# Kernel optimization log

Measured on AMD Instinct MI355X. Metric: run time of the kernel, lower is better.

## Reference

```python
import jax, jax.numpy as jnp
import numpy as np
from jax.scipy.optimize import minimize

LAMDA = 0.01        # lamda default in MI()
N_DOMAINS = 2       # domain_label is binary (source/target)
MAXITER = 50        # BFGS iteration budget (torchmin l-bfgs analogue)


def _sq_dists(A, B):
    # squared euclidean pairwise distances == torch.cdist(A, B, p=2) ** 2
    an = jnp.sum(A * A, axis=-1)
    bn = jnp.sum(B * B, axis=-1)
    return an[:, None] + bn[None, :] - 2.0 * (A @ B.T)


def _median_sigma(sf):
    # sigma = median of nonzero squared pairwise source distances.
    # With continuous features the only zeros are the diagonal, so mask it.
    pd = jnp.maximum(_sq_dists(sf, sf), 0.0)
    pd = jnp.where(jnp.eye(pd.shape[0], dtype=bool), jnp.nan, pd)
    return jnp.nanmedian(pd)


def _build(sf, tf, y, l):
    # Gaussian kernel masked by class agreement, plus domain one-hots.
    sigma = _median_sigma(sf)
    X = jnp.concatenate([sf, tf], axis=0)              # [N, d]
    D = _sq_dists(X, X)                                 # [N, N]
    Deltay = (y[:, None] == y[None, :]).astype(X.dtype)
    K_W = jnp.exp(-D / sigma) * Deltay                  # [N, N]
    onehot = jax.nn.one_hot(l[:, 0], N_DOMAINS, dtype=X.dtype)  # [N, 2]
    KD = K_W * (onehot @ onehot.T)                      # K_W * Deltal
    w = jnp.sum(onehot, axis=0) / X.shape[0]            # domain counts / N
    return K_W, KD, onehot, w


def _div(theta, K_W, KD, onehot, w):
    # mean((K_W*Deltal) @ theta) - mean(exp((theta*K_W) @ Deltal - 1))
    # Deltal = onehot @ onehot.T (rank-2), so the second NxN @ NxN matmul
    # collapses to A = K_W @ (theta[:,None]*onehot) with column weights w.
    term1 = jnp.mean(KD @ theta)
    A = K_W @ (theta[:, None] * onehot)                 # [N, 2]
    term2 = jnp.mean(jnp.exp(A - 1.0) @ w)
    return term1 - term2


def _solve_theta(K_W, KD, onehot, w):
    N = K_W.shape[0]
    obj = lambda th: -_div(th, K_W, KD, onehot, w) + LAMDA * (th @ th)
    res = minimize(obj, jnp.zeros((N,), K_W.dtype), method="BFGS",
                   options={"maxiter": MAXITER})
    return res.x


def setup_inputs() -> dict:
    key = jax.random.key(0)
    k1, k2, k3, k4 = jax.random.split(key, 4)
    B, d, n_class = 2048, 256, 31
    source_features = jax.random.normal(k1, (B, d), dtype=jnp.float32)
    target_features = jax.random.normal(k2, (B, d), dtype=jnp.float32)
    y = jax.random.randint(k3, (2 * B,), 0, n_class, dtype=jnp.int32)
    l = jax.random.randint(k4, (2 * B, 1), 0, N_DOMAINS, dtype=jnp.int32)
    return {"source_features": source_features, "target_features": target_features,
            "y": y, "l": l}


def reference(source_features, target_features, y, l):
    K_W, KD, onehot, w = _build(source_features, target_features, y, l)
    theta_hat = _solve_theta(K_W, KD, onehot, w)
    return _div(theta_hat, K_W, KD, onehot, w)
```

## Files before the change

### kernel.cpp

```cpp
#include <hip/hip_runtime.h>
#include <math.h>

#define N_TOT   4096
#define N_SRC   2048
#define DIMF    256
#define NCLASS  31
#define LAMBDA  0.01f

#define K_TRI1  1048063LL
#define K_TRI2  1048064LL

#define WS_ACC    0
#define WS_HIST0  64
#define WS_HISTA  16448
#define WS_HISTB  32832
#define WS_H2A    49216
#define WS_H2B    50240
#define WS_STATE  51264
#define WS_TICK   51520
#define WS_META   52288
#define WS_SCAL   52800
#define ZERO_BYTES 53248
#define WS_PERM   53248
#define WS_XN     69632
#define WS_DS     1048576
#define WS_KBLK   17825792

#define MAXW 224
#define MAXM 112
#define WPAD 114

__device__ __forceinline__ float bf2f(unsigned short h) {
  return __uint_as_float(((unsigned)h) << 16);
}

__device__ __forceinline__ double blockReduceSum(double v, double* red) {
#pragma unroll
  for (int o = 32; o > 0; o >>= 1) v += __shfl_down(v, o, 64);
  int w = threadIdx.x >> 6, lane = threadIdx.x & 63;
  __syncthreads();
  if (lane == 0) red[w] = v;
  __syncthreads();
  return red[0] + red[1] + red[2] + red[3];
}

__device__ __forceinline__ void blockReduceSumMax(double s, double mx, double* red,
                                                  double& os, double& om) {
#pragma unroll
  for (int o = 32; o > 0; o >>= 1) {
    s += __shfl_down(s, o, 64);
    double u = __shfl_down(mx, o, 64);
    mx = fmax(mx, u);
  }
  int w = threadIdx.x >> 6, lane = threadIdx.x & 63;
  __syncthreads();
  if (lane == 0) { red[w] = s; red[4 + w] = mx; }
  __syncthreads();
  os = red[0] + red[1] + red[2] + red[3];
  om = fmax(fmax(red[4], red[5]), fmax(red[6], red[7]));
}

__device__ void scan_find(const unsigned* hist, int nbins, long long k, unsigned* shOut) {
  __shared__ long long tsum[256];
  int tid = threadIdx.x;
  int per = nbins / 256;
  long long s = 0;
  for (int q = 0; q < per; q++) s += hist[tid * per + q];
  tsum[tid] = s;
  __syncthreads();
  if (tid == 0) {
    long long run = 0;
    for (int t = 0; t < 256; t++) { long long v = tsum[t]; tsum[t] = run; run += v; }
  }
  __syncthreads();
  long long run = tsum[tid];
  for (int q = 0; q < per; q++) {
    unsigned c = hist[tid * per + q];
    if (k >= run && k < run + (long long)c) { shOut[0] = (unsigned)(tid * per + q); shOut[1] = (unsigned)(k - run); }
    run += c;
  }
  __syncthreads();
}

__global__ __launch_bounds__(256) void xn_kernel(const float* __restrict__ sf,
                                                 const float* __restrict__ tf,
                                                 float* __restrict__ xn) {
  int wid = threadIdx.x >> 6, lane = threadIdx.x & 63;
  int row = blockIdx.x * 4 + wid;
  const float* src = (row < N_SRC) ? (sf + (size_t)row * DIMF) : (tf + (size_t)(row - N_SRC) * DIMF);
  float4 v = ((const float4*)src)[lane];
  float s = v.x * v.x + v.y * v.y + v.z * v.z + v.w * v.w;
#pragma unroll
  for (int o = 32; o > 0; o >>= 1) s += __shfl_down(s, o, 64);
  if (lane == 0) xn[row] = s;
}

__global__ __launch_bounds__(256) void dist_k(const float* __restrict__ sf,
                                              const float* __restrict__ xn,
                                              float* __restrict__ Ds,
                                              unsigned* __restrict__ h) {
  __shared__ float As[16][68];
  __shared__ float Bs[16][68];
  __shared__ unsigned lh[4096];
  const int tx = threadIdx.x, ty = threadIdx.y;
  const int tid = ty * 16 + tx;
  for (int q = tid; q < 4096; q += 256) lh[q] = 0;
  int b = blockIdx.x;
  int by = (int)((sqrtf(8.f * (float)b + 1.f) - 1.f) * 0.5f);
  while ((by + 1) * (by + 2) / 2 <= b) ++by;
  while (by * (by + 1) / 2 > b) --by;
  int bx = b - by * (by + 1) / 2;
  const int R = by * 64, C = bx * 64;
  const int si = tid >> 2, sq = tid & 3;
  float4 va = ((const float4*)(sf + (size_t)(R + si) * 256 + 0))[sq];
  float4 vb = ((const float4*)(sf + (size_t)(C + si) * 256 + 0))[sq];
  float acc[4][4] = {};
  for (int kc = 0; kc < 256; kc += 16) {
    As[sq * 4 + 0][si] = va.x; As[sq * 4 + 1][si] = va.y; As[sq * 4 + 2][si] = va.z; As[sq * 4 + 3][si] = va.w;
    Bs[sq * 4 + 0][si] = vb.x; Bs[sq * 4 + 1][si] = vb.y; Bs[sq * 4 + 2][si] = vb.z; Bs[sq * 4 + 3][si] = vb.w;
    __syncthreads();
    if (kc + 16 < 256) {
      va = ((const float4*)(sf + (size_t)(R + si) * 256 + kc + 16))[sq];
      vb = ((const float4*)(sf + (size_t)(C + si) * 256 + kc + 16))[sq];
    }
#pragma unroll
    for (int k = 0; k < 16; k++) {
      float4 a = *(const float4*)&As[k][ty * 4];
      float4 b2 = *(const float4*)&Bs[k][tx * 4];
      acc[0][0] += a.x * b2.x; acc[0][1] += a.x * b2.y; acc[0][2] += a.x * b2.z; acc[0][3] += a.x * b2.w;
      acc[1][0] += a.y * b2.x; acc[1][1] += a.y * b2.y; acc[1][2] += a.y * b2.z; acc[1][3] += a.y * b2.w;
      acc[2][0] += a.z * b2.x; acc[2][1] += a.z * b2.y; acc[2][2] += a.z * b2.z; acc[2][3] += a.z * b2.w;
      acc[3][0] += a.w * b2.x; acc[3][1] += a.w * b2.y; acc[3][2] += a.w * b2.z; acc[3][3] += a.w * b2.w;
    }
    __syncthreads();
  }
  int jbase = C + tx * 4;
  float xnj0 = xn[jbase + 0], xnj1 = xn[jbase + 1], xnj2 = xn[jbase + 2], xnj3 = xn[jbase + 3];
#pragma unroll
  for (int r = 0; r < 4; r++) {
    int i = R + ty * 4 + r;
    float xni = xn[i];
    float v[4];
    v[0] = fmaxf(xni + xnj0 - 2.f * acc[r][0], 0.f);
    v[1] = fmaxf(xni + xnj1 - 2.f * acc[r][1], 0.f);
    v[2] = fmaxf(xni + xnj2 - 2.f * acc[r][2], 0.f);
    v[3] = fmaxf(xni + xnj3 - 2.f * acc[r][3], 0.f);
    if (jbase + 3 < i) {
      float4 o; o.x = v[0]; o.y = v[1]; o.z = v[2]; o.w = v[3];
      ((float4*)&Ds[(size_t)i * 2048 + jbase])[0] = o;
      atomicAdd(&lh[__float_as_uint(v[0]) >> 20], 1u);
      atomicAdd(&lh[__float_as_uint(v[1]) >> 20], 1u);
      atomicAdd(&lh[__float_as_uint(v[2]) >> 20], 1u);
      atomicAdd(&lh[__float_as_uint(v[3]) >> 20], 1u);
    } else {
#pragma unroll
      for (int k = 0; k < 4; k++) {
        if (jbase + k < i) {
          Ds[(size_t)i * 2048 + jbase + k] = v[k];
          atomicAdd(&lh[__float_as_uint(v[k]) >> 20], 1u);
        }
      }
    }
  }
  __syncthreads();
  for (int q = tid; q < 4096; q += 256) if (lh[q]) atomicAdd(&h[q], lh[q]);
}

__global__ __launch_bounds__(256) void scan0_k(const unsigned* __restrict__ h, unsigned* __restrict__ st) {
  __shared__ unsigned r0[2];
  __shared__ unsigned r1[2];
  scan_find(h, 4096, K_TRI1, r0);
  scan_find(h, 4096, K_TRI2, r1);
  if (threadIdx.x == 0) { st[0] = r0[0]; st[1] = r0[1]; st[2] = r1[0]; st[3] = r1[1]; }
}

__global__ __launch_bounds__(256) void hist1_k(const float* __restrict__ Ds, const unsigned* __restrict__ st,
                                               unsigned* __restrict__ hA, unsigned* __restrict__ hB) {
  __shared__ unsigned lA[4096];
  __shared__ unsigned lB[4096];
  for (int i = threadIdx.x; i < 4096; i += 256) { lA[i] = 0; lB[i] = 0; }
  __syncthreads();
  unsigned s0 = st[0], s1 = st[2];
  int gw = (blockIdx.x * 256 + threadIdx.x) >> 6;
  int lane = threadIdx.x & 63;
  const float* row = Ds + (size_t)gw * 2048;
  for (int j = lane; j < gw; j += 64) {
    unsigned u = __float_as_uint(row[j]);
    unsigned hi = u >> 20, mid = (u >> 8) & 0xFFFu;
    if (hi == s0) atomicAdd(&lA[mid], 1u);
    if (hi == s1) atomicAdd(&lB[mid], 1u);
  }
  __syncthreads();
  for (int i = threadIdx.x; i < 4096; i += 256) {
    if (lA[i]) atomicAdd(&hA[i], lA[i]);
    if (lB[i]) atomicAdd(&hB[i], lB[i]);
  }
}

__global__ __launch_bounds__(256) void scan1_k(const unsigned* __restrict__ hA, const unsigned* __restrict__ hB,
                                               unsigned* __restrict__ st) {
  __shared__ unsigned r0[2];
  __shared__ unsigned r1[2];
  long long kA = (long long)st[1];
  long long kB = (long long)st[3];
  scan_find(hA, 4096, kA, r0);
  scan_find(hB, 4096, kB, r1);
  if (threadIdx.x == 0) { st[4] = r0[0]; st[5] = r0[1]; st[6] = r1[0]; st[7] = r1[1]; }
}

__global__ __launch_bounds__(256) void hist2_k(const float* __restrict__ Ds, const unsigned* __restrict__ st,
                                               unsigned* __restrict__ hA, unsigned* __restrict__ hB) {
  __shared__ unsigned lA[256];
  __shared__ unsigned lB[256];
  lA[threadIdx.x] = 0; lB[threadIdx.x] = 0;
  __syncthreads();
  unsigned p0 = (st[0] << 12) | st[4];
  unsigned p1 = (st[2] << 12) | st[6];
  int gw = (blockIdx.x * 256 + threadIdx.x) >> 6;
  int lane = threadIdx.x & 63;
  const float* row = Ds + (size_t)gw * 2048;
  for (int j = lane; j < gw; j += 64) {
    unsigned u = __float_as_uint(row[j]);
    unsigned pre = u >> 8;
    if (pre == p0) atomicAdd(&lA[u & 0xFFu], 1u);
    if (pre == p1) atomicAdd(&lB[u & 0xFFu], 1u);
  }
  __syncthreads();
  if (lA[threadIdx.x]) atomicAdd(&hA[threadIdx.x], lA[threadIdx.x]);
  if (lB[threadIdx.x]) atomicAdd(&hB[threadIdx.x], lB[threadIdx.x]);
}

__global__ __launch_bounds__(256) void scan2b_k(const unsigned* __restrict__ hA, const unsigned* __restrict__ hB,
                                                const unsigned* __restrict__ st, float* __restrict__ scal,
                                                const int* __restrict__ y, const int* __restrict__ l,
                                                int* __restrict__ perm, int* __restrict__ meta) {
  int tid = threadIdx.x;
  __shared__ unsigned r0[2];
  __shared__ unsigned r1[2];
  scan_find(hA, 256, (long long)st[5], r0);
  scan_find(hB, 256, (long long)st[7], r1);
  if (tid == 0) {
    unsigned v1 = (st[0] << 20) | (st[4] << 8) | r0[0];
    unsigned v2 = (st[2] << 20) | (st[6] << 8) | r1[0];
    scal[0] = 0.5f * (__uint_as_float(v1) + __uint_as_float(v2));
  }
  __shared__ unsigned cl[64];
  __shared__ unsigned bs2[64];
  __shared__ unsigned cur[64];
  if (tid < 64) cl[tid] = 0;
  __syncthreads();
  for (int i = tid; i < N_TOT; i += 256) atomicAdd(&cl[y[i] * 2 + l[i]], 1u);
  __syncthreads();
  if (tid == 0) {
    unsigned run = 0;
    for (int b2 = 0; b2 < 62; b2++) { bs2[b2] = run; run += cl[b2]; }
    unsigned run2 = 0, cnt0 = 0;
    for (int c = 0; c < NCLASS; c++) {
      int n = (int)(cl[2 * c] + cl[2 * c + 1]);
      meta[c] = n; meta[32 + c] = (int)cl[2 * c]; meta[64 + c] = (int)bs2[2 * c];
      meta[96 + c] = (int)run2; run2 += (unsigned)(n * n);
      cnt0 += cl[2 * c];
    }
    scal[1] = (float)((double)cnt0 / (4096.0 * 4096.0));
    scal[2] = (float)((double)(N_TOT - cnt0) / (4096.0 * 4096.0));
  }
  __syncthreads();
  if (tid < 64) cur[tid] = bs2[tid];
  __syncthreads();
  for (int i = tid; i < N_TOT; i += 256) {
    int b2 = y[i] * 2 + l[i];
    unsigned pos = atomicAdd(&cur[b2], 1u);
    perm[pos] = i;
  }
}

__global__ __launch_bounds__(256) void build_k(const float* __restrict__ sf, const float* __restrict__ tf,
                                               const float* __restrict__ xn, const int* __restrict__ perm,
                                               const int* __restrict__ meta, const float* __restrict__ scal,
                                               float* __restrict__ gK) {
  const int c = blockIdx.z;
  const int n = meta[c];
  const int cs = meta[64 + c];
  const int bo = meta[96 + c];
  const int T = (n + 15) >> 4;
  int b = blockIdx.x;
  if (b >= T * (T + 1) / 2) return;
  int by = (int)((sqrtf(8.f * (float)b + 1.f) - 1.f) * 0.5f);
  while ((by + 1) * (by + 2) / 2 <= b) ++by;
  while (by * (by + 1) / 2 > b) --by;
  int bx = b - by * (by + 1) / 2;
  const int i0 = by * 16, j0 = bx * 16;
  const int tx = threadIdx.x, ty = threadIdx.y;
  __shared__ float As[16][260];
  __shared__ float Bs[16][260];
  __shared__ float ot[16][17];
  __shared__ int ra[16];
  __shared__ int rb[16];
  int tid = ty * 16 + tx;
  if (tid < 16) { int il = i0 + tid; ra[tid] = (il < n) ? perm[cs + il] : -1; }
  else if (tid < 32) { int jl = j0 + tid - 16; rb[tid - 16] = (jl < n) ? perm[cs + jl] : -1; }
  __syncthreads();
  for (int e = tid; e < 1024; e += 256) {
    int r = e >> 6, q = e & 63;
    int g = ra[r];
    if (g >= 0) {
      const float* src = (g < N_SRC) ? (sf + (size_t)g * DIMF) : (tf + (size_t)(g - N_SRC) * DIMF);
      ((float4*)&As[r][q * 4])[0] = ((const float4*)src)[q];
    }
    int g2 = rb[r];
    if (g2 >= 0) {
      const float* src = (g2 < N_SRC) ? (sf + (size_t)g2 * DIMF) : (tf + (size_t)(g2 - N_SRC) * DIMF);
      ((float4*)&Bs[r][q * 4])[0] = ((const float4*)src)[q];
    }
  }
  __syncthreads();
  int il = i0 + ty, jl = j0 + tx;
  float val = 0.f;
  if (il < n && jl < n) {
    float dot = 0.f;
    const float4* a4 = (const float4*)&As[ty][0];
    const float4* b4 = (const float4*)&Bs[tx][0];
#pragma unroll 16
    for (int q = 0; q < 64; q++) {
      float4 a = a4[q], b2 = b4[q];
      dot += a.x * b2.x + a.y * b2.y + a.z * b2.z + a.w * b2.w;
    }
    int gi = ra[ty], gj = rb[tx];
    float d = xn[gi] + xn[gj] - 2.f * dot;
    val = expf(-d / scal[0]);
    gK[(size_t)bo + (size_t)il * n + jl] = val;
  }
  ot[ty][tx] = val;
  __syncthreads();
  if (by != bx) {
    int il2 = j0 + ty, jl2 = i0 + tx;
    if (il2 < n && jl2 < n) gK[(size_t)bo + (size_t)il2 * n + jl2] = ot[tx][ty];
  }
}

__global__ __launch_bounds__(256) void solver_k(const float* __restrict__ gK, const int* __restrict__ meta,
                                                const float* __restrict__ scal, double* __restrict__ acc,
                                                unsigned* __restrict__ tick, float* __restrict__ out) {
  const int c = blockIdx.x >> 1, d = blockIdx.x & 1;
  const int n = meta[c];
  const int m0 = meta[32 + c];
  const int m = d ? (n - m0) : m0;
  const int c0 = d ? m0 : 0;
  const int bo = meta[96 + c];
  const float gamma = scal[1 + d];
  const int tid = threadIdx.x;
  const int wv = tid >> 6, lane = tid & 63;

  __shared__ unsigned short Wl[MAXW * WPAD];
  __shared__ float pS[4 * MAXM];
  __shared__ float pD[4 * MAXM];
  __shared__ float Av[MAXW];
  __shared__ float Sv[MAXW];
  __shared__ float Uv[MAXW];
  __shared__ float Bq[MAXW];
  __shared__ float bc[MAXM];
  __shared__ float th[MAXM + 1];
  __shared__ float gv[MAXM];
  __shared__ float dgv[MAXM];
  __shared__ float pv[MAXM + 1];
  __shared__ float rv[MAXM + 1];
  __shared__ float zv[MAXM + 1];
  __shared__ float xv[MAXM + 1];
  __shared__ double red[16];

  const float* K = gK + bo;
  const int st = n;
  const int mp2 = (m + 1) & ~1;
  const int iw0 = (n * wv) >> 2, iw1 = (n * (wv + 1)) >> 2;

  for (int i = tid >> 2; i < n; i += 64) {
    const float* Kr = K + (size_t)i * st + c0;
    unsigned short* Wr = Wl + i * WPAD;
    for (int j = (tid & 3); j < m; j += 4) {
      unsigned u = __float_as_uint(Kr[j]);
      u += 0x7fffu + ((u >> 16) & 1u);
      Wr[j] = (unsigned short)(u >> 16);
    }
    if ((tid & 3) == 0 && (m & 1)) Wr[m] = 0;
  }
  {
    const int r0 = (m * wv) >> 2, r1 = (m * (wv + 1)) >> 2;
    for (int j = lane; j < m; j += 64) {
      const float* Kr = K + (size_t)(c0 + j) * st + c0;
      float s = 0.f;
      for (int r = r0; r < r1; r++) s += Kr[r];
      pS[wv * MAXM + j] = s;
    }
  }
  __syncthreads();
  for (int j = tid; j < mp2; j += 256) {
    if (j < m) bc[j] = (pS[j] + pS[MAXM + j] + pS[2 * MAXM + j] + pS[3 * MAXM + j]) * (1.0f / 4096.0f);
    th[j] = 0.f;
  }
  __syncthreads();

  for (int it = 0; it < 25; it++) {
    double o = 0.0;
    if (it == 0) {
      const float s0c = gamma * expf(-1.f);
      for (int i = tid; i < n; i += 256) { Av[i] = 0.f; Sv[i] = s0c; o += (double)s0c; }
    } else {
      for (int i = tid; i < n; i += 256) {
        const unsigned short* Wr = Wl + i * WPAD;
        float a = 0.f;
#pragma unroll 4
        for (int j = 0; j < mp2; j += 2) {
          unsigned u = *(const unsigned*)(Wr + j);
          a += __uint_as_float(u << 16) * th[j]
             + __uint_as_float(u & 0xffff0000u) * th[j + 1];
        }
        Av[i] = a;
      }
      __syncthreads();
      for (int i = tid; i < n; i += 256) {
        float si = gamma * expf(fminf(Av[i] - 1.f, 30.f));
        Sv[i] = si; o += (double)si;
      }
      for (int j = tid; j < m; j += 256) {
        float t_ = th[j];
        o += (double)(-bc[j] * t_ + LAMBDA * t_ * t_);
      }
    }
    __syncthreads();
    if (it == 0) {
      for (int j = lane; j < m; j += 64) {
        const unsigned short* Wc = Wl + j;
        float s_ = 0.f, ds_ = 0.f;
        int i = iw0;
        for (; i + 3 < iw1; i += 4) {
          float w0 = bf2f(Wc[(i + 0) * WPAD]), w1 = bf2f(Wc[(i + 1) * WPAD]);
          float w2 = bf2f(Wc[(i + 2) * WPAD]), w3 = bf2f(Wc[(i + 3) * WPAD]);
          float a0 = w0 * Sv[i], a1 = w1 * Sv[i + 1], a2 = w2 * Sv[i + 2], a3 = w3 * Sv[i + 3];
          s_ += a0 + a1 + a2 + a3;
          ds_ += a0 * w0 + a1 * w1 + a2 * w2 + a3 * w3;
        }
        for (; i < iw1; i++) { float w = bf2f(Wc[i * WPAD]); float a = w * Sv[i]; s_ += a; ds_ += a * w; }
        pS[wv * MAXM + j] = s_; pD[wv * MAXM + j] = ds_;
      }
    } else {
      for (int j = lane; j < m; j += 64) {
        const unsigned short* Wc = Wl + j;
        float s_ = 0.f;
        int i = iw0;
        for (; i + 3 < iw1; i += 4)
          s_ += bf2f(Wc[(i+0)*WPAD]) * Sv[i]   + bf2f(Wc[(i+1)*WPAD]) * Sv[i+1]
              + bf2f(Wc[(i+2)*WPAD]) * Sv[i+2] + bf2f(Wc[(i+3)*WPAD]) * Sv[i+3];
        for (; i < iw1; i++) s_ += bf2f(Wc[i * WPAD]) * Sv[i];
        pS[wv * MAXM + j] = s_;
      }
    }
    __syncthreads();
    double gm = 0.0;
    for (int j = tid; j < m; j += 256) {
      float s_ = pS[j] + pS[MAXM + j] + pS[2 * MAXM + j] + pS[3 * MAXM + j];
      if (it == 0) {
        float ds_ = pD[j] + pD[MAXM + j] + pD[2 * MAXM + j] + pD[3 * MAXM + j];
        dgv[j] = ds_ + 2.f * LAMBDA;
      }
      float g = s_ - bc[j] + 2.f * LAMBDA * th[j];
      gv[j] = g;
      double ag = fabs((double)g); if (ag > gm) gm = ag;
    }
    double obj, gmax;
    blockReduceSumMax(o, gm, red, obj, gmax);
    if (gmax < 1e-5) break;

    const double tolf = (it == 0) ? 1e-2 : ((it == 1) ? 1e-3 : 1e-4);
    double rz = 0.0;
    for (int j = tid; j < mp2; j += 256) {
      float r0 = (j < m) ? -gv[j] : 0.f;
      float z0 = (j < m) ? r0 / dgv[j] : 0.f;
      rv[j] = r0; zv[j] = z0; pv[j] = z0; xv[j] = 0.f;
      rz += (double)r0 * (double)z0;
    }
    rz = blockReduceSum(rz, red);
    double rz0 = rz;
    for (int cg = 0; cg < 12; cg++) {
      __syncthreads();
      for (int i = tid; i < n; i += 256) {
        const unsigned short* Wr = Wl + i * WPAD;
        float a = 0.f;
#pragma unroll 4
        for (int j = 0; j < mp2; j += 2) {
          unsigned u = *(const unsigned*)(Wr + j);
          a += __uint_as_float(u << 16) * pv[j]
             + __uint_as_float(u & 0xffff0000u) * pv[j + 1];
        }
        Uv[i] = a * Sv[i];
      }
      __syncthreads();
      for (int j = lane; j < m; j += 64) {
        const unsigned short* Wc = Wl + j;
        float q = 0.f;
        int i = iw0;
        for (; i + 3 < iw1; i += 4)
          q += bf2f(Wc[(i+0)*WPAD]) * Uv[i]   + bf2f(Wc[(i+1)*WPAD]) * Uv[i+1]
             + bf2f(Wc[(i+2)*WPAD]) * Uv[i+2] + bf2f(Wc[(i+3)*WPAD]) * Uv[i+3];
        for (; i < iw1; i++) q += bf2f(Wc[i * WPAD]) * Uv[i];
        pS[wv * MAXM + j] = q;
      }
      __syncthreads();
      double pq = 0.0;
      for (int j = tid; j < m; j += 256) {
        float q = pS[j] + pS[MAXM + j] + pS[2 * MAXM + j] + pS[3 * MAXM + j] + 2.f * LAMBDA * pv[j];
        Bq[j] = q;
        pq += (double)pv[j] * (double)q;
      }
      pq = blockReduceSum(pq, red);
      if (!(pq > 0.0)) break;
      float alpha = (float)(rz / pq);
      double rznew = 0.0;
      for (int j = tid; j < m; j += 256) {
        xv[j] += alpha * pv[j];
        float rn = rv[j] - alpha * Bq[j];
        rv[j] = rn;
        float zn = rn / dgv[j];
        zv[j] = zn;
        rznew += (double)rn * (double)zn;
      }
      rznew = blockReduceSum(rznew, red);
      if (rznew < tolf * rz0 || cg == 11) break;
      float beta = (float)(rznew / rz);
      for (int j = tid; j < m; j += 256) pv[j] = zv[j] + beta * pv[j];
      rz = rznew;
    }
    __syncthreads();
    double gtpl = 0.0, pml = 0.0;
    for (int j = tid; j < m; j += 256) {
      gtpl += (double)gv[j] * (double)xv[j];
      double ax = fabs((double)xv[j]); if (ax > pml) pml = ax;
    }
    double gtp, pmax;
    blockReduceSumMax(gtpl, pml, red, gtp, pmax);
    if (!(gtp < 0.0)) break;

    float t = 1.f;
    if (-gtp >= 1e-4) {
      for (int i = tid; i < n; i += 256) {
        const unsigned short* Wr = Wl + i * WPAD;
        float a = 0.f;
#pragma unroll 4
        for (int j = 0; j < mp2; j += 2) {
          unsigned u = *(const unsigned*)(Wr + j);
          a += __uint_as_float(u << 16) * xv[j]
             + __uint_as_float(u & 0xffff0000u) * xv[j + 1];
        }
        Bq[i] = a;
      }
      __syncthreads();
      for (int ls = 0; ls < 10; ls++) {
        double ol = 0.0;
        for (int i = tid; i < n; i += 256)
          ol += (double)(gamma * expf(fminf(Av[i] + t * Bq[i] - 1.f, 30.f)));
        for (int j = tid; j < m; j += 256) {
          float tj = th[j] + t * xv[j];
          ol += (double)(-bc[j] * tj + LAMBDA * tj * tj);
        }
        double ot2 = blockReduceSum(ol, red);
        if (ot2 <= obj + 1e-4 * (double)t * gtp) break;
        t *= 0.5f;
      }
    }
    for (int j = tid; j < mp2; j += 256) th[j] += t * xv[j];
    __syncthreads();
    if ((double)t * pmax < 1e-7) break;
  }

  __syncthreads();
  for (int i = tid; i < n; i += 256) {
    const float* Kr = K + (size_t)i * st + c0;
    float a = 0.f;
    int j = 0;
    for (; j + 7 < m; j += 8)
      a += th[j] * Kr[j] + th[j+1] * Kr[j+1] + th[j+2] * Kr[j+2] + th[j+3] * Kr[j+3]
         + th[j+4] * Kr[j+4] + th[j+5] * Kr[j+5] + th[j+6] * Kr[j+6] + th[j+7] * Kr[j+7];
    for (; j < m; j++) a += th[j] * Kr[j];
    Av[i] = a;
  }
  __syncthreads();
  double t1l = 0.0, t2l = 0.0;
  for (int i = tid; i < n; i += 256) t2l += (double)(gamma * expf(fminf(Av[i] - 1.f, 30.f)));
  for (int j = tid; j < m; j += 256) t1l += (double)(bc[j] * th[j]);
  double t1 = blockReduceSum(t1l, red);
  double t2 = blockReduceSum(t2l, red);
  if (tid == 0) {
    atomicAdd(&acc[0], t1);
    atomicAdd(&acc[1], t2);
    __threadfence();
    unsigned old = __hip_atomic_fetch_add(&tick[0], 1u, __ATOMIC_ACQ_REL, __HIP_MEMORY_SCOPE_AGENT);
    if (old == 61u) {
      double a0 = __hip_atomic_load(&acc[0], __ATOMIC_RELAXED, __HIP_MEMORY_SCOPE_AGENT);
      double a1 = __hip_atomic_load(&acc[1], __ATOMIC_RELAXED, __HIP_MEMORY_SCOPE_AGENT);
      out[0] = (float)(a0 - a1);
    }
  }
}

extern "C" void kernel_launch(void* const* d_in, const int* in_sizes, int n_in,
                              void* d_out, int out_size, void* d_ws, size_t ws_size,
                              hipStream_t stream) {
  const float* sf = (const float*)d_in[0];
  const float* tf = (const float*)d_in[1];
  const int* y = (const int*)d_in[2];
  const int* l = (const int*)d_in[3];
  char* ws = (char*)d_ws;

  double*   acc    = (double*)(ws + WS_ACC);
  unsigned* hist0  = (unsigned*)(ws + WS_HIST0);
  unsigned* histA  = (unsigned*)(ws + WS_HISTA);
  unsigned* histB  = (unsigned*)(ws + WS_HISTB);
  unsigned* h2A    = (unsigned*)(ws + WS_H2A);
  unsigned* h2B    = (unsigned*)(ws + WS_H2B);
  unsigned* state  = (unsigned*)(ws + WS_STATE);
  unsigned* tick   = (unsigned*)(ws + WS_TICK);
  int*      meta   = (int*)(ws + WS_META);
  float*    scal   = (float*)(ws + WS_SCAL);
  int*      perm   = (int*)(ws + WS_PERM);
  float*    xnp    = (float*)(ws + WS_XN);
  float*    Ds     = (float*)(ws + WS_DS);
  float*    gK     = (float*)(ws + WS_KBLK);

  hipMemsetAsync(d_ws, 0, ZERO_BYTES, stream);
  hipLaunchKernelGGL(xn_kernel, dim3(1024), dim3(256), 0, stream, sf, tf, xnp);
  hipLaunchKernelGGL(dist_k, dim3(528), dim3(16, 16), 0, stream, sf, xnp, Ds, hist0);
  hipLaunchKernelGGL(scan0_k, dim3(1), dim3(256), 0, stream, hist0, state);
  hipLaunchKernelGGL(hist1_k, dim3(512), dim3(256), 0, stream, Ds, state, histA, histB);
  hipLaunchKernelGGL(scan1_k, dim3(1), dim3(256), 0, stream, histA, histB, state);
  hipLaunchKernelGGL(hist2_k, dim3(512), dim3(256), 0, stream, Ds, state, h2A, h2B);
  hipLaunchKernelGGL(scan2b_k, dim3(1), dim3(256), 0, stream, h2A, h2B, state, scal, y, l, perm, meta);
  hipLaunchKernelGGL(build_k, dim3(105, 1, NCLASS), dim3(16, 16), 0, stream, sf, tf, xnp, perm, meta, scal, gK);
  hipLaunchKernelGGL(solver_k, dim3(62), dim3(256), 0, stream, gK, meta, scal, acc, tick, (float*)d_out);
}
```

Measured before the change: 232.5 us.

## Fuse radix-select refinement passes and shrink solver blocks to two waves

```diff
diff --git a/kernel.cpp b/kernel.cpp
--- a/kernel.cpp
+++ b/kernel.cpp
@@ -14,8 +14,6 @@
 #define WS_HIST0  64
 #define WS_HISTA  16448
 #define WS_HISTB  32832
-#define WS_H2A    49216
-#define WS_H2B    50240
 #define WS_STATE  51264
 #define WS_TICK   51520
 #define WS_META   52288
@@ -25,6 +23,8 @@
 #define WS_XN     69632
 #define WS_DS     1048576
 #define WS_KBLK   17825792
+#define WS_BIGA   17825792
+#define WS_BIGB   22020096
 
 #define MAXW 224
 #define MAXM 112
@@ -34,18 +34,18 @@
   return __uint_as_float(((unsigned)h) << 16);
 }
 
-__device__ __forceinline__ double blockReduceSum(double v, double* red) {
+__device__ __forceinline__ double blockReduceSum2(double v, double* red) {
 #pragma unroll
   for (int o = 32; o > 0; o >>= 1) v += __shfl_down(v, o, 64);
   int w = threadIdx.x >> 6, lane = threadIdx.x & 63;
   __syncthreads();
   if (lane == 0) red[w] = v;
   __syncthreads();
-  return red[0] + red[1] + red[2] + red[3];
-}
-
-__device__ __forceinline__ void blockReduceSumMax(double s, double mx, double* red,
-                                                  double& os, double& om) {
+  return red[0] + red[1];
+}
+
+__device__ __forceinline__ void blockReduceSumMax2(double s, double mx, double* red,
+                                                   double& os, double& om) {
 #pragma unroll
   for (int o = 32; o > 0; o >>= 1) {
     s += __shfl_down(s, o, 64);
@@ -56,8 +56,8 @@
   __syncthreads();
   if (lane == 0) { red[w] = s; red[4 + w] = mx; }
   __syncthreads();
-  os = red[0] + red[1] + red[2] + red[3];
-  om = fmax(fmax(red[4], red[5]), fmax(red[6], red[7]));
+  os = red[0] + red[1];
+  om = fmax(red[4], red[5]);
 }
 
 __device__ void scan_find(const unsigned* hist, int nbins, long long k, unsigned* shOut) {
@@ -98,12 +98,17 @@
 __global__ __launch_bounds__(256) void dist_k(const float* __restrict__ sf,
                                               const float* __restrict__ xn,
                                               float* __restrict__ Ds,
-                                              unsigned* __restrict__ h) {
+                                              unsigned* __restrict__ h,
+                                              uint4* __restrict__ bigz) {
   __shared__ float As[16][68];
   __shared__ float Bs[16][68];
   __shared__ unsigned lh[4096];
   const int tx = threadIdx.x, ty = threadIdx.y;
   const int tid = ty * 16 + tx;
+  {
+    uint4 z; z.x = 0; z.y = 0; z.z = 0; z.w = 0;
+    for (int q = blockIdx.x * 256 + tid; q < 524288; q += 135168) bigz[q] = z;
+  }
   for (int q = tid; q < 4096; q += 256) lh[q] = 0;
   int b = blockIdx.x;
   int by = (int)((sqrtf(8.f * (float)b + 1.f) - 1.f) * 0.5f);
@@ -175,7 +180,8 @@
 }
 
 __global__ __launch_bounds__(256) void hist1_k(const float* __restrict__ Ds, const unsigned* __restrict__ st,
-                                               unsigned* __restrict__ hA, unsigned* __restrict__ hB) {
+                                               unsigned* __restrict__ hA, unsigned* __restrict__ hB,
+                                               unsigned* __restrict__ bigA, unsigned* __restrict__ bigB) {
   __shared__ unsigned lA[4096];
   __shared__ unsigned lB[4096];
   for (int i = threadIdx.x; i < 4096; i += 256) { lA[i] = 0; lB[i] = 0; }
@@ -187,8 +193,8 @@
   for (int j = lane; j < gw; j += 64) {
     unsigned u = __float_as_uint(row[j]);
     unsigned hi = u >> 20, mid = (u >> 8) & 0xFFFu;
-    if (hi == s0) atomicAdd(&lA[mid], 1u);
-    if (hi == s1) atomicAdd(&lB[mid], 1u);
+    if (hi == s0) { atomicAdd(&lA[mid], 1u); atomicAdd(&bigA[u & 0xFFFFFu], 1u); }
+    if (hi == s1) { atomicAdd(&lB[mid], 1u); atomicAdd(&bigB[u & 0xFFFFFu], 1u); }
   }
   __syncthreads();
   for (int i = threadIdx.x; i < 4096; i += 256) {
@@ -197,51 +203,20 @@
   }
 }
 
-__global__ __launch_bounds__(256) void scan1_k(const unsigned* __restrict__ hA, const unsigned* __restrict__ hB,
-                                               unsigned* __restrict__ st) {
-  __shared__ unsigned r0[2];
-  __shared__ unsigned r1[2];
-  long long kA = (long long)st[1];
-  long long kB = (long long)st[3];
-  scan_find(hA, 4096, kA, r0);
-  scan_find(hB, 4096, kB, r1);
-  if (threadIdx.x == 0) { st[4] = r0[0]; st[5] = r0[1]; st[6] = r1[0]; st[7] = r1[1]; }
-}
-
-__global__ __launch_bounds__(256) void hist2_k(const float* __restrict__ Ds, const unsigned* __restrict__ st,
-                                               unsigned* __restrict__ hA, unsigned* __restrict__ hB) {
-  __shared__ unsigned lA[256];
-  __shared__ unsigned lB[256];
-  lA[threadIdx.x] = 0; lB[threadIdx.x] = 0;
-  __syncthreads();
-  unsigned p0 = (st[0] << 12) | st[4];
-  unsigned p1 = (st[2] << 12) | st[6];
-  int gw = (blockIdx.x * 256 + threadIdx.x) >> 6;
-  int lane = threadIdx.x & 63;
-  const float* row = Ds + (size_t)gw * 2048;
-  for (int j = lane; j < gw; j += 64) {
-    unsigned u = __float_as_uint(row[j]);
-    unsigned pre = u >> 8;
-    if (pre == p0) atomicAdd(&lA[u & 0xFFu], 1u);
-    if (pre == p1) atomicAdd(&lB[u & 0xFFu], 1u);
-  }
-  __syncthreads();
-  if (lA[threadIdx.x]) atomicAdd(&hA[threadIdx.x], lA[threadIdx.x]);
-  if (lB[threadIdx.x]) atomicAdd(&hB[threadIdx.x], lB[threadIdx.x]);
-}
-
-__global__ __launch_bounds__(256) void scan2b_k(const unsigned* __restrict__ hA, const unsigned* __restrict__ hB,
-                                                const unsigned* __restrict__ st, float* __restrict__ scal,
-                                                const int* __restrict__ y, const int* __restrict__ l,
-                                                int* __restrict__ perm, int* __restrict__ meta) {
+__global__ __launch_bounds__(256) void scanF_k(const unsigned* __restrict__ hA, const unsigned* __restrict__ hB,
+                                               const unsigned* __restrict__ bigA, const unsigned* __restrict__ bigB,
+                                               const unsigned* __restrict__ st, float* __restrict__ scal,
+                                               const int* __restrict__ y, const int* __restrict__ l,
+                                               int* __restrict__ perm, int* __restrict__ meta) {
   int tid = threadIdx.x;
-  __shared__ unsigned r0[2];
-  __shared__ unsigned r1[2];
-  scan_find(hA, 256, (long long)st[5], r0);
-  scan_find(hB, 256, (long long)st[7], r1);
+  __shared__ unsigned m0[2], m1[2], l0[2], l1[2];
+  scan_find(hA, 4096, (long long)st[1], m0);
+  scan_find(hB, 4096, (long long)st[3], m1);
+  scan_find(bigA + (size_t)m0[0] * 256, 256, (long long)m0[1], l0);
+  scan_find(bigB + (size_t)m1[0] * 256, 256, (long long)m1[1], l1);
   if (tid == 0) {
-    unsigned v1 = (st[0] << 20) | (st[4] << 8) | r0[0];
-    unsigned v2 = (st[2] << 20) | (st[6] << 8) | r1[0];
+    unsigned v1 = (st[0] << 20) | (m0[0] << 8) | l0[0];
+    unsigned v2 = (st[2] << 20) | (m1[0] << 8) | l1[0];
     scal[0] = 0.5f * (__uint_as_float(v1) + __uint_as_float(v2));
   }
   __shared__ unsigned cl[64];
@@ -338,7 +313,7 @@
   }
 }
 
-__global__ __launch_bounds__(256) void solver_k(const float* __restrict__ gK, const int* __restrict__ meta,
+__global__ __launch_bounds__(128) void solver_k(const float* __restrict__ gK, const int* __restrict__ meta,
                                                 const float* __restrict__ scal, double* __restrict__ acc,
                                                 unsigned* __restrict__ tick, float* __restrict__ out) {
   const int c = blockIdx.x >> 1, d = blockIdx.x & 1;
@@ -352,8 +327,8 @@
   const int wv = tid >> 6, lane = tid & 63;
 
   __shared__ unsigned short Wl[MAXW * WPAD];
-  __shared__ float pS[4 * MAXM];
-  __shared__ float pD[4 * MAXM];
+  __shared__ float pS[2 * MAXM];
+  __shared__ float pD[2 * MAXM];
   __shared__ float Av[MAXW];
   __shared__ float Sv[MAXW];
   __shared__ float Uv[MAXW];
@@ -366,15 +341,15 @@
   __shared__ float rv[MAXM + 1];
   __shared__ float zv[MAXM + 1];
   __shared__ float xv[MAXM + 1];
-  __shared__ double red[16];
+  __shared__ double red[8];
 
   const float* K = gK + bo;
-  const int st = n;
+  const int st2 = n;
   const int mp2 = (m + 1) & ~1;
-  const int iw0 = (n * wv) >> 2, iw1 = (n * (wv + 1)) >> 2;
-
-  for (int i = tid >> 2; i < n; i += 64) {
-    const float* Kr = K + (size_t)i * st + c0;
+  const int iw0 = (n * wv) >> 1, iw1 = (n * (wv + 1)) >> 1;
+
+  for (int i = tid >> 2; i < n; i += 32) {
+    const float* Kr = K + (size_t)i * st2 + c0;
     unsigned short* Wr = Wl + i * WPAD;
     for (int j = (tid & 3); j < m; j += 4) {
       unsigned u = __float_as_uint(Kr[j]);
@@ -384,17 +359,17 @@
     if ((tid & 3) == 0 && (m & 1)) Wr[m] = 0;
   }
   {
-    const int r0 = (m * wv) >> 2, r1 = (m * (wv + 1)) >> 2;
+    const int r0 = (m * wv) >> 1, r1 = (m * (wv + 1)) >> 1;
     for (int j = lane; j < m; j += 64) {
-      const float* Kr = K + (size_t)(c0 + j) * st + c0;
+      const float* Kr = K + (size_t)(c0 + j) * st2 + c0;
       float s = 0.f;
       for (int r = r0; r < r1; r++) s += Kr[r];
       pS[wv * MAXM + j] = s;
     }
   }
   __syncthreads();
-  for (int j = tid; j < mp2; j += 256) {
-    if (j < m) bc[j] = (pS[j] + pS[MAXM + j] + pS[2 * MAXM + j] + pS[3 * MAXM + j]) * (1.0f / 4096.0f);
+  for (int j = tid; j < mp2; j += 128) {
+    if (j < m) bc[j] = (pS[j] + pS[MAXM + j]) * (1.0f / 4096.0f);
     th[j] = 0.f;
   }
   __syncthreads();
@@ -403,9 +378,9 @@
     double o = 0.0;
     if (it == 0) {
       const float s0c = gamma * expf(-1.f);
-      for (int i = tid; i < n; i += 256) { Av[i] = 0.f; Sv[i] = s0c; o += (double)s0c; }
+      for (int i = tid; i < n; i += 128) { Av[i] = 0.f; Sv[i] = s0c; o += (double)s0c; }
     } else {
-      for (int i = tid; i < n; i += 256) {
+      for (int i = tid; i < n; i += 128) {
         const unsigned short* Wr = Wl + i * WPAD;
         float a = 0.f;
 #pragma unroll 4
@@ -417,11 +392,11 @@
         Av[i] = a;
       }
       __syncthreads();
-      for (int i = tid; i < n; i += 256) {
+      for (int i = tid; i < n; i += 128) {
         float si = gamma * expf(fminf(Av[i] - 1.f, 30.f));
         Sv[i] = si; o += (double)si;
       }
-      for (int j = tid; j < m; j += 256) {
+      for (int j = tid; j < m; j += 128) {
         float t_ = th[j];
         o += (double)(-bc[j] * t_ + LAMBDA * t_ * t_);
       }
@@ -456,33 +431,30 @@
     }
     __syncthreads();
     double gm = 0.0;
-    for (int j = tid; j < m; j += 256) {
-      float s_ = pS[j] + pS[MAXM + j] + pS[2 * MAXM + j] + pS[3 * MAXM + j];
-      if (it == 0) {
-        float ds_ = pD[j] + pD[MAXM + j] + pD[2 * MAXM + j] + pD[3 * MAXM + j];
-        dgv[j] = ds_ + 2.f * LAMBDA;
-      }
+    for (int j = tid; j < m; j += 128) {
+      float s_ = pS[j] + pS[MAXM + j];
+      if (it == 0) dgv[j] = pD[j] + pD[MAXM + j] + 2.f * LAMBDA;
       float g = s_ - bc[j] + 2.f * LAMBDA * th[j];
       gv[j] = g;
       double ag = fabs((double)g); if (ag > gm) gm = ag;
     }
     double obj, gmax;
-    blockReduceSumMax(o, gm, red, obj, gmax);
+    blockReduceSumMax2(o, gm, red, obj, gmax);
     if (gmax < 1e-5) break;
 
     const double tolf = (it == 0) ? 1e-2 : ((it == 1) ? 1e-3 : 1e-4);
     double rz = 0.0;
-    for (int j = tid; j < mp2; j += 256) {
+    for (int j = tid; j < mp2; j += 128) {
       float r0 = (j < m) ? -gv[j] : 0.f;
       float z0 = (j < m) ? r0 / dgv[j] : 0.f;
       rv[j] = r0; zv[j] = z0; pv[j] = z0; xv[j] = 0.f;
       rz += (double)r0 * (double)z0;
     }
-    rz = blockReduceSum(rz, red);
+    rz = blockReduceSum2(rz, red);
     double rz0 = rz;
     for (int cg = 0; cg < 12; cg++) {
       __syncthreads();
-      for (int i = tid; i < n; i += 256) {
+      for (int i = tid; i < n; i += 128) {
         const unsigned short* Wr = Wl + i * WPAD;
         float a = 0.f;
 #pragma unroll 4
@@ -506,16 +478,16 @@
       }
       __syncthreads();
       double pq = 0.0;
-      for (int j = tid; j < m; j += 256) {
-        float q = pS[j] + pS[MAXM + j] + pS[2 * MAXM + j] + pS[3 * MAXM + j] + 2.f * LAMBDA * pv[j];
+      for (int j = tid; j < m; j += 128) {
+        float q = pS[j] + pS[MAXM + j] + 2.f * LAMBDA * pv[j];
         Bq[j] = q;
         pq += (double)pv[j] * (double)q;
       }
-      pq = blockReduceSum(pq, red);
+      pq = blockReduceSum2(pq, red);
       if (!(pq > 0.0)) break;
       float alpha = (float)(rz / pq);
       double rznew = 0.0;
-      for (int j = tid; j < m; j += 256) {
+      for (int j = tid; j < m; j += 128) {
         xv[j] += alpha * pv[j];
         float rn = rv[j] - alpha * Bq[j];
         rv[j] = rn;
@@ -523,25 +495,25 @@
         zv[j] = zn;
         rznew += (double)rn * (double)zn;
       }
-      rznew = blockReduceSum(rznew, red);
+      rznew = blockReduceSum2(rznew, red);
       if (rznew < tolf * rz0 || cg == 11) break;
       float beta = (float)(rznew / rz);
-      for (int j = tid; j < m; j += 256) pv[j] = zv[j] + beta * pv[j];
+      for (int j = tid; j < m; j += 128) pv[j] = zv[j] + beta * pv[j];
       rz = rznew;
     }
     __syncthreads();
     double gtpl = 0.0, pml = 0.0;
-    for (int j = tid; j < m; j += 256) {
+    for (int j = tid; j < m; j += 128) {
       gtpl += (double)gv[j] * (double)xv[j];
       double ax = fabs((double)xv[j]); if (ax > pml) pml = ax;
     }
     double gtp, pmax;
-    blockReduceSumMax(gtpl, pml, red, gtp, pmax);
+    blockReduceSumMax2(gtpl, pml, red, gtp, pmax);
     if (!(gtp < 0.0)) break;
 
     float t = 1.f;
     if (-gtp >= 1e-4) {
-      for (int i = tid; i < n; i += 256) {
+      for (int i = tid; i < n; i += 128) {
         const unsigned short* Wr = Wl + i * WPAD;
         float a = 0.f;
 #pragma unroll 4
@@ -555,25 +527,25 @@
       __syncthreads();
       for (int ls = 0; ls < 10; ls++) {
         double ol = 0.0;
-        for (int i = tid; i < n; i += 256)
+        for (int i = tid; i < n; i += 128)
           ol += (double)(gamma * expf(fminf(Av[i] + t * Bq[i] - 1.f, 30.f)));
-        for (int j = tid; j < m; j += 256) {
+        for (int j = tid; j < m; j += 128) {
           float tj = th[j] + t * xv[j];
           ol += (double)(-bc[j] * tj + LAMBDA * tj * tj);
         }
-        double ot2 = blockReduceSum(ol, red);
+        double ot2 = blockReduceSum2(ol, red);
         if (ot2 <= obj + 1e-4 * (double)t * gtp) break;
         t *= 0.5f;
       }
     }
-    for (int j = tid; j < mp2; j += 256) th[j] += t * xv[j];
+    for (int j = tid; j < mp2; j += 128) th[j] += t * xv[j];
     __syncthreads();
     if ((double)t * pmax < 1e-7) break;
   }
 
   __syncthreads();
-  for (int i = tid; i < n; i += 256) {
-    const float* Kr = K + (size_t)i * st + c0;
+  for (int i = tid; i < n; i += 128) {
+    const float* Kr = K + (size_t)i * st2 + c0;
     float a = 0.f;
     int j = 0;
     for (; j + 7 < m; j += 8)
@@ -584,10 +556,10 @@
   }
   __syncthreads();
   double t1l = 0.0, t2l = 0.0;
-  for (int i = tid; i < n; i += 256) t2l += (double)(gamma * expf(fminf(Av[i] - 1.f, 30.f)));
-  for (int j = tid; j < m; j += 256) t1l += (double)(bc[j] * th[j]);
-  double t1 = blockReduceSum(t1l, red);
-  double t2 = blockReduceSum(t2l, red);
+  for (int i = tid; i < n; i += 128) t2l += (double)(gamma * expf(fminf(Av[i] - 1.f, 30.f)));
+  for (int j = tid; j < m; j += 128) t1l += (double)(bc[j] * th[j]);
+  double t1 = blockReduceSum2(t1l, red);
+  double t2 = blockReduceSum2(t2l, red);
   if (tid == 0) {
     atomicAdd(&acc[0], t1);
     atomicAdd(&acc[1], t2);
@@ -614,8 +586,6 @@
   unsigned* hist0  = (unsigned*)(ws + WS_HIST0);
   unsigned* histA  = (unsigned*)(ws + WS_HISTA);
   unsigned* histB  = (unsigned*)(ws + WS_HISTB);
-  unsigned* h2A    = (unsigned*)(ws + WS_H2A);
-  unsigned* h2B    = (unsigned*)(ws + WS_H2B);
   unsigned* state  = (unsigned*)(ws + WS_STATE);
   unsigned* tick   = (unsigned*)(ws + WS_TICK);
   int*      meta   = (int*)(ws + WS_META);
@@ -623,16 +593,16 @@
   int*      perm   = (int*)(ws + WS_PERM);
   float*    xnp    = (float*)(ws + WS_XN);
   float*    Ds     = (float*)(ws + WS_DS);
+  unsigned* bigA   = (unsigned*)(ws + WS_BIGA);
+  unsigned* bigB   = (unsigned*)(ws + WS_BIGB);
   float*    gK     = (float*)(ws + WS_KBLK);
 
   hipMemsetAsync(d_ws, 0, ZERO_BYTES, stream);
   hipLaunchKernelGGL(xn_kernel, dim3(1024), dim3(256), 0, stream, sf, tf, xnp);
-  hipLaunchKernelGGL(dist_k, dim3(528), dim3(16, 16), 0, stream, sf, xnp, Ds, hist0);
+  hipLaunchKernelGGL(dist_k, dim3(528), dim3(16, 16), 0, stream, sf, xnp, Ds, hist0, (uint4*)bigA);
   hipLaunchKernelGGL(scan0_k, dim3(1), dim3(256), 0, stream, hist0, state);
-  hipLaunchKernelGGL(hist1_k, dim3(512), dim3(256), 0, stream, Ds, state, histA, histB);
-  hipLaunchKernelGGL(scan1_k, dim3(1), dim3(256), 0, stream, histA, histB, state);
-  hipLaunchKernelGGL(hist2_k, dim3(512), dim3(256), 0, stream, Ds, state, h2A, h2B);
-  hipLaunchKernelGGL(scan2b_k, dim3(1), dim3(256), 0, stream, h2A, h2B, state, scal, y, l, perm, meta);
+  hipLaunchKernelGGL(hist1_k, dim3(512), dim3(256), 0, stream, Ds, state, histA, histB, bigA, bigB);
+  hipLaunchKernelGGL(scanF_k, dim3(1), dim3(256), 0, stream, histA, histB, bigA, bigB, state, scal, y, l, perm, meta);
   hipLaunchKernelGGL(build_k, dim3(105, 1, NCLASS), dim3(16, 16), 0, stream, sf, tf, xnp, perm, meta, scal, gK);
-  hipLaunchKernelGGL(solver_k, dim3(62), dim3(256), 0, stream, gK, meta, scal, acc, tick, (float*)d_out);
-}
+  hipLaunchKernelGGL(solver_k, dim3(62), dim3(128), 0, stream, gK, meta, scal, acc, tick, (float*)d_out);
+}
```

New measurement: 296.7 us. 27.6% more time.

## Widen distance tile K-chunk, fuse exp into matvec, derive g·p from CG

Applied to the files above, without the earlier changes.

```diff
diff --git a/kernel.cpp b/kernel.cpp
--- a/kernel.cpp
+++ b/kernel.cpp
@@ -99,8 +99,8 @@
                                               const float* __restrict__ xn,
                                               float* __restrict__ Ds,
                                               unsigned* __restrict__ h) {
-  __shared__ float As[16][68];
-  __shared__ float Bs[16][68];
+  __shared__ float As[64][68];
+  __shared__ float Bs[64][68];
   __shared__ unsigned lh[4096];
   const int tx = threadIdx.x, ty = threadIdx.y;
   const int tid = ty * 16 + tx;
@@ -112,19 +112,30 @@
   int bx = b - by * (by + 1) / 2;
   const int R = by * 64, C = bx * 64;
   const int si = tid >> 2, sq = tid & 3;
-  float4 va = ((const float4*)(sf + (size_t)(R + si) * 256 + 0))[sq];
-  float4 vb = ((const float4*)(sf + (size_t)(C + si) * 256 + 0))[sq];
+  float4 va[4], vb[4];
+#pragma unroll
+  for (int qq = 0; qq < 4; qq++) {
+    va[qq] = ((const float4*)(sf + (size_t)(R + si) * 256))[sq + qq * 4];
+    vb[qq] = ((const float4*)(sf + (size_t)(C + si) * 256))[sq + qq * 4];
+  }
   float acc[4][4] = {};
-  for (int kc = 0; kc < 256; kc += 16) {
-    As[sq * 4 + 0][si] = va.x; As[sq * 4 + 1][si] = va.y; As[sq * 4 + 2][si] = va.z; As[sq * 4 + 3][si] = va.w;
-    Bs[sq * 4 + 0][si] = vb.x; Bs[sq * 4 + 1][si] = vb.y; Bs[sq * 4 + 2][si] = vb.z; Bs[sq * 4 + 3][si] = vb.w;
+  for (int kc = 0; kc < 256; kc += 64) {
+#pragma unroll
+    for (int qq = 0; qq < 4; qq++) {
+      int kb = (sq + qq * 4) * 4;
+      As[kb + 0][si] = va[qq].x; As[kb + 1][si] = va[qq].y; As[kb + 2][si] = va[qq].z; As[kb + 3][si] = va[qq].w;
+      Bs[kb + 0][si] = vb[qq].x; Bs[kb + 1][si] = vb[qq].y; Bs[kb + 2][si] = vb[qq].z; Bs[kb + 3][si] = vb[qq].w;
+    }
     __syncthreads();
-    if (kc + 16 < 256) {
-      va = ((const float4*)(sf + (size_t)(R + si) * 256 + kc + 16))[sq];
-      vb = ((const float4*)(sf + (size_t)(C + si) * 256 + kc + 16))[sq];
-    }
-#pragma unroll
-    for (int k = 0; k < 16; k++) {
+    if (kc + 64 < 256) {
+#pragma unroll
+      for (int qq = 0; qq < 4; qq++) {
+        va[qq] = ((const float4*)(sf + (size_t)(R + si) * 256 + kc + 64))[sq + qq * 4];
+        vb[qq] = ((const float4*)(sf + (size_t)(C + si) * 256 + kc + 64))[sq + qq * 4];
+      }
+    }
+#pragma unroll 16
+    for (int k = 0; k < 64; k++) {
       float4 a = *(const float4*)&As[k][ty * 4];
       float4 b2 = *(const float4*)&Bs[k][tx * 4];
       acc[0][0] += a.x * b2.x; acc[0][1] += a.x * b2.y; acc[0][2] += a.x * b2.z; acc[0][3] += a.x * b2.w;
@@ -415,10 +426,7 @@
              + __uint_as_float(u & 0xffff0000u) * th[j + 1];
         }
         Av[i] = a;
-      }
-      __syncthreads();
-      for (int i = tid; i < n; i += 256) {
-        float si = gamma * expf(fminf(Av[i] - 1.f, 30.f));
+        float si = gamma * expf(fminf(a - 1.f, 30.f));
         Sv[i] = si; o += (double)si;
       }
       for (int j = tid; j < m; j += 256) {
@@ -480,6 +488,7 @@
     }
     rz = blockReduceSum(rz, red);
     double rz0 = rz;
+    double gtpacc = 0.0;
     for (int cg = 0; cg < 12; cg++) {
       __syncthreads();
       for (int i = tid; i < n; i += 256) {
@@ -514,6 +523,7 @@
       pq = blockReduceSum(pq, red);
       if (!(pq > 0.0)) break;
       float alpha = (float)(rz / pq);
+      gtpacc += (double)alpha * rz;
       double rznew = 0.0;
       for (int j = tid; j < m; j += 256) {
         xv[j] += alpha * pv[j];
@@ -530,13 +540,7 @@
       rz = rznew;
     }
     __syncthreads();
-    double gtpl = 0.0, pml = 0.0;
-    for (int j = tid; j < m; j += 256) {
-      gtpl += (double)gv[j] * (double)xv[j];
-      double ax = fabs((double)xv[j]); if (ax > pml) pml = ax;
-    }
-    double gtp, pmax;
-    blockReduceSumMax(gtpl, pml, red, gtp, pmax);
+    double gtp = -gtpacc;
     if (!(gtp < 0.0)) break;
 
     float t = 1.f;
@@ -568,7 +572,6 @@
     }
     for (int j = tid; j < mp2; j += 256) th[j] += t * xv[j];
     __syncthreads();
-    if ((double)t * pmax < 1e-7) break;
   }
 
   __syncthreads();
```

New measurement: 238.4 us. 2.5% more time.
